# Kernel tuning notes

Measured on AMD Instinct MI355X. Metric: run time of the kernel, lower is better.

## Reference

```python
import jax, jax.numpy as jnp
import numpy as np

N_NODES = 100000
N_EDGES = 1000000
IN_FEATS = 128
HIDDEN = 256


def setup_inputs() -> dict:
    key = jax.random.key(0)
    ks = jax.random.split(key, 8)
    h_src_nodes = jax.random.normal(ks[0], (N_NODES, IN_FEATS), dtype=jnp.float32)
    h_dst_nodes = jax.random.normal(ks[1], (N_NODES, IN_FEATS), dtype=jnp.float32)
    src = jax.random.randint(ks[2], (N_EDGES,), 0, N_NODES, dtype=jnp.int32)
    dst = jax.random.randint(ks[3], (N_EDGES,), 0, N_NODES, dtype=jnp.int32)
    # MLP params, stored as [in, out] so forward is x @ W + b
    s1 = 1.0 / np.sqrt(2 * IN_FEATS)
    s2 = 1.0 / np.sqrt(HIDDEN)
    W1 = jax.random.uniform(ks[4], (2 * IN_FEATS, HIDDEN), jnp.float32, -s1, s1)
    b1 = jax.random.uniform(ks[5], (HIDDEN,), jnp.float32, -s1, s1)
    W2 = jax.random.uniform(ks[6], (HIDDEN, 1), jnp.float32, -s2, s2)
    b2 = jax.random.uniform(ks[7], (1,), jnp.float32, -s2, s2)
    return {"h_src_nodes": h_src_nodes, "h_dst_nodes": h_dst_nodes,
            "src": src, "dst": dst, "W1": W1, "b1": b1, "W2": W2, "b2": b2}


def reference(h_src_nodes, h_dst_nodes, src, dst, W1, b1, W2, b2):
    # gather endpoint features per edge, concat -> [E, 2*in_feats]
    h_cat = jnp.concatenate([h_src_nodes[src], h_dst_nodes[dst]], axis=1)
    hidden = jax.nn.relu(h_cat @ W1 + b1)        # [E, hidden]
    score = (hidden @ W2 + b2).squeeze(-1)        # [E]
    return score
```

## Files before the change

kernel.cpp:

```cpp
#include <hip/hip_runtime.h>
#include <hip/hip_bf16.h>
#include <stdint.h>

#define IN_FEATS 128
#define HID 256

typedef __bf16   bf16x8 __attribute__((ext_vector_type(8)));
typedef float    f32x4  __attribute__((ext_vector_type(4)));
typedef _Float16 h2     __attribute__((ext_vector_type(2)));
typedef _Float16 h8     __attribute__((ext_vector_type(8)));

__global__ void k_prep(const float* __restrict__ W1, const float* __restrict__ W2,
                       __bf16* __restrict__ W1P, _Float16* __restrict__ W2H) {
    int t = blockIdx.x * 256 + threadIdx.x;
    if (t < 8192) {
        int lane  = t & 63;
        int nblk  = (t >> 6) & 15;
        int ks    = (t >> 10) & 3;
        int which = (t >> 12) & 1;
        int qr = lane & 15, qg = lane >> 4;
        int n  = nblk * 16 + qr;
        int k0 = which * 128 + ks * 32 + qg * 8;
        bf16x8 v;
#pragma unroll
        for (int j = 0; j < 8; ++j)
            v[j] = (__bf16)W1[(size_t)(k0 + j) * HID + n];
        *(bf16x8*)(W1P + (size_t)t * 8) = v;
    } else {
        int i = t - 8192;
        if (i < HID) W2H[i] = (_Float16)W2[i];
    }
}

__global__ __launch_bounds__(256) void k_proj(
    const float* __restrict__ hs, const float* __restrict__ hd,
    const __bf16* __restrict__ W1P, const float* __restrict__ b1,
    _Float16* __restrict__ Ps, _Float16* __restrict__ Pd)
{
    const int which = blockIdx.y;
    const float* __restrict__ h = which ? hd : hs;
    _Float16* __restrict__ P = which ? Pd : Ps;

    const int lane = threadIdx.x & 63;
    const int w    = threadIdx.x >> 6;
    const int n0   = w * 64;
    const int node0 = blockIdx.x * 32;
    const int qr = lane & 15;
    const int qg = lane >> 4;
    const bf16x8* __restrict__ W1Pv = (const bf16x8*)W1P;

    f32x4 acc[2][4];
#pragma unroll
    for (int m = 0; m < 2; ++m)
#pragma unroll
        for (int n = 0; n < 4; ++n) acc[m][n] = (f32x4){0.f, 0.f, 0.f, 0.f};

#pragma unroll
    for (int ks = 0; ks < 4; ++ks) {
        const int k0 = ks * 32 + qg * 8;
        bf16x8 a[2];
#pragma unroll
        for (int m = 0; m < 2; ++m) {
            const float* ap = h + (size_t)(node0 + m * 16 + qr) * IN_FEATS + k0;
            float4 f0 = *(const float4*)ap;
            float4 f1 = *(const float4*)(ap + 4);
            bf16x8 t;
            t[0] = (__bf16)f0.x; t[1] = (__bf16)f0.y; t[2] = (__bf16)f0.z; t[3] = (__bf16)f0.w;
            t[4] = (__bf16)f1.x; t[5] = (__bf16)f1.y; t[6] = (__bf16)f1.z; t[7] = (__bf16)f1.w;
            a[m] = t;
        }
#pragma unroll
        for (int n = 0; n < 4; ++n) {
            bf16x8 b = W1Pv[((size_t)(which * 4 + ks) * 16 + w * 4 + n) * 64 + lane];
#pragma unroll
            for (int m = 0; m < 2; ++m)
                acc[m][n] = __builtin_amdgcn_mfma_f32_16x16x32_bf16(a[m], b, acc[m][n], 0, 0, 0);
        }
    }

    const bool even = (qr & 1) == 0;
    const int i0 = even ? 0 : 2;
#pragma unroll
    for (int n = 0; n < 4; ++n) {
        const int col = n0 + n * 16 + qr;
        const float bias = which ? 0.f : b1[col];
#pragma unroll
        for (int m = 0; m < 2; ++m) {
            const int rowb = node0 + m * 16 + qg * 4;
            float v[4], o[4];
#pragma unroll
            for (int i = 0; i < 4; ++i) {
                v[i] = acc[m][n][i] + bias;
                o[i] = __shfl_xor(v[i], 1, 64);
            }
#pragma unroll
            for (int i = 0; i < 2; ++i) {
                const int r = i0 + i;
                auto pk = even ? __builtin_amdgcn_cvt_pkrtz(v[r], o[r])
                               : __builtin_amdgcn_cvt_pkrtz(o[r], v[r]);
                *(unsigned*)(P + (size_t)(rowb + r) * HID + (col & ~1)) =
                    __builtin_bit_cast(unsigned, pk);
            }
        }
    }
}

__device__ __forceinline__ float dot8f(h8 a, h8 c, h8 w, float acc) {
    h8 r = a + c;
    r = __builtin_elementwise_max(r, (h8)(_Float16)0.f);
#pragma unroll
    for (int j = 0; j < 4; ++j) {
        h2 p = {r[2 * j], r[2 * j + 1]};
        h2 q = {w[2 * j], w[2 * j + 1]};
        acc = __builtin_amdgcn_fdot2(p, q, acc, false);
    }
    return acc;
}

__global__ __launch_bounds__(256) void k_edge(
    const _Float16* __restrict__ Ps, const _Float16* __restrict__ Pd,
    const int* __restrict__ src, const int* __restrict__ dst,
    const _Float16* __restrict__ W2H, const float* __restrict__ b2,
    float* __restrict__ out, int e_beg, int e_end)
{
    const int lane = threadIdx.x & 63;
    const int q = lane & 15;
    const int g = lane >> 4;
    const int wave = blockIdx.x * 4 + (threadIdx.x >> 6);
    const int nw = gridDim.x * 4;

    const h8* __restrict__ W2v = (const h8*)W2H;
    const h8 wa0 = W2v[q];
    const h8 wa1 = W2v[16 + q];
    const float bias = b2[0];

    for (int base = e_beg + wave * 8; base < e_end; base += nw * 8) {
        const int e0 = base + g;
        const int e1 = base + 4 + g;
        const bool v0 = (e0 < e_end), v1 = (e1 < e_end);
        float acc0 = 0.f, acc1 = 0.f;
        if (v0) {
            const h8* ps = (const h8*)(Ps + (size_t)src[e0] * HID);
            const h8* pd = (const h8*)(Pd + (size_t)dst[e0] * HID);
            h8 a0 = ps[q], a1 = ps[16 + q], c0 = pd[q], c1 = pd[16 + q];
            if (v1) {
                const h8* ps1 = (const h8*)(Ps + (size_t)src[e1] * HID);
                const h8* pd1 = (const h8*)(Pd + (size_t)dst[e1] * HID);
                h8 b0 = ps1[q], b1v = ps1[16 + q], d0 = pd1[q], d1 = pd1[16 + q];
                acc0 = dot8f(a0, c0, wa0, acc0);
                acc0 = dot8f(a1, c1, wa1, acc0);
                acc1 = dot8f(b0, d0, wa0, acc1);
                acc1 = dot8f(b1v, d1, wa1, acc1);
            } else {
                acc0 = dot8f(a0, c0, wa0, acc0);
                acc0 = dot8f(a1, c1, wa1, acc0);
            }
        }
#pragma unroll
        for (int m = 1; m < 16; m <<= 1) {
            acc0 += __shfl_xor(acc0, m, 64);
            acc1 += __shfl_xor(acc1, m, 64);
        }
        if (q == 0) {
            if (v0) out[e0] = acc0 + bias;
            if (v1) out[e1] = acc1 + bias;
        }
    }
}

extern "C" void kernel_launch(void* const* d_in, const int* in_sizes, int n_in,
                              void* d_out, int out_size, void* d_ws, size_t ws_size,
                              hipStream_t stream) {
    const float* h_src = (const float*)d_in[0];
    const float* h_dst = (const float*)d_in[1];
    const int*   src   = (const int*)d_in[2];
    const int*   dst   = (const int*)d_in[3];
    const float* W1    = (const float*)d_in[4];
    const float* b1    = (const float*)d_in[5];
    const float* W2    = (const float*)d_in[6];
    const float* b2    = (const float*)d_in[7];
    float* out = (float*)d_out;

    const int E  = in_sizes[2];
    const int NN = in_sizes[0] / IN_FEATS;

    __bf16*    W1P = (__bf16*)d_ws;
    _Float16*  W2H = (_Float16*)((char*)d_ws + 131072);
    _Float16*  Ps  = (_Float16*)((char*)d_ws + 262144);
    _Float16*  Pd  = Ps + (size_t)NN * HID;

    k_prep<<<33, 256, 0, stream>>>(W1, W2, W1P, W2H);
    dim3 gA(NN / 32, 2);
    k_proj<<<gA, 256, 0, stream>>>(h_src, h_dst, W1P, b1, Ps, Pd);
    const int Eh = E / 2;
    k_edge<<<2048, 256, 0, stream>>>(Ps, Pd, src, dst, W2H, b2, out, 0, Eh);
    k_edge<<<2048, 256, 0, stream>>>(Ps, Pd, src, dst, W2H, b2, out, Eh, E);
}
```

Baseline: 346.4 us.

## Stage node feature tile in LDS and double rows per projection block

```diff
diff --git a/kernel.cpp b/kernel.cpp
--- a/kernel.cpp
+++ b/kernel.cpp
@@ -4,7 +4,10 @@
 
 #define IN_FEATS 128
 #define HID 256
-
+#define BM 64
+#define LDA 136
+
+typedef __bf16   bf16x4 __attribute__((ext_vector_type(4)));
 typedef __bf16   bf16x8 __attribute__((ext_vector_type(8)));
 typedef float    f32x4  __attribute__((ext_vector_type(4)));
 typedef _Float16 h2     __attribute__((ext_vector_type(2)));
@@ -35,45 +38,54 @@
 __global__ __launch_bounds__(256) void k_proj(
     const float* __restrict__ hs, const float* __restrict__ hd,
     const __bf16* __restrict__ W1P, const float* __restrict__ b1,
-    _Float16* __restrict__ Ps, _Float16* __restrict__ Pd)
+    _Float16* __restrict__ Ps, _Float16* __restrict__ Pd, int NN)
 {
+    __shared__ __bf16 Atile[BM][LDA];
+
     const int which = blockIdx.y;
     const float* __restrict__ h = which ? hd : hs;
     _Float16* __restrict__ P = which ? Pd : Ps;
 
-    const int lane = threadIdx.x & 63;
-    const int w    = threadIdx.x >> 6;
-    const int n0   = w * 64;
-    const int node0 = blockIdx.x * 32;
+    const int lane  = threadIdx.x & 63;
+    const int w     = threadIdx.x >> 6;
+    const int n0    = w * 64;
+    const int node0 = blockIdx.x * BM;
     const int qr = lane & 15;
     const int qg = lane >> 4;
     const bf16x8* __restrict__ W1Pv = (const bf16x8*)W1P;
 
-    f32x4 acc[2][4];
-#pragma unroll
-    for (int m = 0; m < 2; ++m)
+    {
+        const int t = threadIdx.x;
+#pragma unroll
+        for (int j = 0; j < 8; ++j) {
+            int g   = t + 256 * j;
+            int row = g >> 5;
+            int c4  = (g & 31) * 4;
+            int rsrc = node0 + row; if (rsrc > NN - 1) rsrc = NN - 1;
+            float4 f = *(const float4*)(h + (size_t)rsrc * IN_FEATS + c4);
+            bf16x4 v = { (__bf16)f.x, (__bf16)f.y, (__bf16)f.z, (__bf16)f.w };
+            *(bf16x4*)&Atile[row][c4] = v;
+        }
+    }
+    __syncthreads();
+
+    f32x4 acc[4][4];
+#pragma unroll
+    for (int m = 0; m < 4; ++m)
 #pragma unroll
         for (int n = 0; n < 4; ++n) acc[m][n] = (f32x4){0.f, 0.f, 0.f, 0.f};
 
 #pragma unroll
     for (int ks = 0; ks < 4; ++ks) {
-        const int k0 = ks * 32 + qg * 8;
-        bf16x8 a[2];
-#pragma unroll
-        for (int m = 0; m < 2; ++m) {
-            const float* ap = h + (size_t)(node0 + m * 16 + qr) * IN_FEATS + k0;
-            float4 f0 = *(const float4*)ap;
-            float4 f1 = *(const float4*)(ap + 4);
-            bf16x8 t;
-            t[0] = (__bf16)f0.x; t[1] = (__bf16)f0.y; t[2] = (__bf16)f0.z; t[3] = (__bf16)f0.w;
-            t[4] = (__bf16)f1.x; t[5] = (__bf16)f1.y; t[6] = (__bf16)f1.z; t[7] = (__bf16)f1.w;
-            a[m] = t;
-        }
+        bf16x8 a[4];
+#pragma unroll
+        for (int m = 0; m < 4; ++m)
+            a[m] = *(const bf16x8*)&Atile[m * 16 + qr][ks * 32 + qg * 8];
 #pragma unroll
         for (int n = 0; n < 4; ++n) {
             bf16x8 b = W1Pv[((size_t)(which * 4 + ks) * 16 + w * 4 + n) * 64 + lane];
 #pragma unroll
-            for (int m = 0; m < 2; ++m)
+            for (int m = 0; m < 4; ++m)
                 acc[m][n] = __builtin_amdgcn_mfma_f32_16x16x32_bf16(a[m], b, acc[m][n], 0, 0, 0);
         }
     }
@@ -85,8 +97,8 @@
         const int col = n0 + n * 16 + qr;
         const float bias = which ? 0.f : b1[col];
 #pragma unroll
-        for (int m = 0; m < 2; ++m) {
-            const int rowb = node0 + m * 16 + qg * 4;
+        for (int m = 0; m < 4; ++m) {
+            const int rowb = m * 16 + qg * 4;
             float v[4], o[4];
 #pragma unroll
             for (int i = 0; i < 4; ++i) {
@@ -96,10 +108,12 @@
 #pragma unroll
             for (int i = 0; i < 2; ++i) {
                 const int r = i0 + i;
-                auto pk = even ? __builtin_amdgcn_cvt_pkrtz(v[r], o[r])
-                               : __builtin_amdgcn_cvt_pkrtz(o[r], v[r]);
-                *(unsigned*)(P + (size_t)(rowb + r) * HID + (col & ~1)) =
-                    __builtin_bit_cast(unsigned, pk);
+                if (node0 + rowb + r < NN) {
+                    auto pk = even ? __builtin_amdgcn_cvt_pkrtz(v[r], o[r])
+                                   : __builtin_amdgcn_cvt_pkrtz(o[r], v[r]);
+                    *(unsigned*)(P + (size_t)(node0 + rowb + r) * HID + (col & ~1)) =
+                        __builtin_bit_cast(unsigned, pk);
+                }
             }
         }
     }
@@ -190,8 +204,8 @@
     _Float16*  Pd  = Ps + (size_t)NN * HID;
 
     k_prep<<<33, 256, 0, stream>>>(W1, W2, W1P, W2H);
-    dim3 gA(NN / 32, 2);
-    k_proj<<<gA, 256, 0, stream>>>(h_src, h_dst, W1P, b1, Ps, Pd);
+    dim3 gA((NN + BM - 1) / BM, 2);
+    k_proj<<<gA, 256, 0, stream>>>(h_src, h_dst, W1P, b1, Ps, Pd, NN);
     const int Eh = E / 2;
     k_edge<<<2048, 256, 0, stream>>>(Ps, Pd, src, dst, W2H, b2, out, 0, Eh);
     k_edge<<<2048, 256, 0, stream>>>(Ps, Pd, src, dst, W2H, b2, out, Eh, E);
```

Measured after the change: 313.9 us. 1.1x faster.
